# Kernel optimization log

Hardware: AMD Instinct MI355X
Metric: run time of the kernel (lower is better)

Reference implementation:

```python
import jax, jax.numpy as jnp
import numpy as np

B, MAX_N, MAX_E, MAX_BETA = 16, 512, 1024, 64
NODE_F, HID = 2, 128

def setup_inputs() -> dict:
    key = jax.random.key(0)
    ks = jax.random.split(key, 20)
    inp = {}
    inp["x"] = jax.random.normal(ks[0], (B, MAX_N, NODE_F), dtype=jnp.float32)
    inp["SCB"] = jax.random.normal(ks[1], (B, MAX_BETA, MAX_E), dtype=jnp.float32)
    inp["edge_index"] = jax.random.randint(ks[2], (B, 2, MAX_E), 0, MAX_N, dtype=jnp.int32)
    inp["edge_len"] = jax.random.randint(ks[3], (B,), 1, MAX_E + 1, dtype=jnp.int32)
    inp["beta_len"] = jax.random.randint(ks[4], (B,), 1, MAX_BETA + 1, dtype=jnp.int32)
    def lin(k, fi, fo):
        s = 1.0 / np.sqrt(fi)
        kw, kb = jax.random.split(k)
        return (jax.random.uniform(kw, (fi, fo), jnp.float32, -s, s),
                jax.random.uniform(kb, (fo,), jnp.float32, -s, s))
    inp["W1"], inp["b1"] = lin(ks[5], 4, 64)
    inp["W2"], inp["b2"] = lin(ks[6], 64, 64)
    inp["W3"], inp["b3"] = lin(ks[7], 64 + 4, 128)
    inp["W4"], inp["b4"] = lin(ks[8], 128, 128)
    inp["W5"], inp["b5"] = lin(ks[9], 128, HID)
    inp["W6"], inp["b6"] = lin(ks[10], HID, HID)
    return inp

def reference(x, SCB, edge_index, edge_len, beta_len,
              W1, b1, W2, b2, W3, b3, W4, b4, W5, b5, W6, b6):
    Bb, beta, E = SCB.shape
    SCBa = jnp.abs(SCB)  # torch.abs(he[2].to_dense())
    edge_mask = jnp.arange(E)[None, :] < edge_len[:, None]      # [B,E]
    beta_mask = jnp.arange(beta)[None, :] < beta_len[:, None]   # [B,beta]
    # e_feat = x[edge_index].transpose(0,1).reshape(E, 2*node_feat)
    ef = jax.vmap(lambda xi, ei: xi[ei])(x, edge_index)          # [B,2,E,F]
    ef = jnp.transpose(ef, (0, 2, 1, 3)).reshape(Bb, E, -1)      # [B,E,4]
    # SCB_feat[b,beta,e,i] = e_feat[b,e,i] * SCB[b,beta,e]; zero in padded region
    valid = (beta_mask[:, :, None] & edge_mask[:, None, :])[..., None]
    SCB_feat = jnp.where(valid, SCBa[:, :, :, None] * ef[:, None, :, :], 0.0)  # [B,beta,E,4]
    L1 = jnp.transpose(SCB_feat, (0, 2, 1, 3))                   # [B,E,beta,4]
    # SCB_encoder on sum over edges
    s = L1.sum(axis=1)                                            # [B,beta,4]
    emb = jax.nn.relu(s @ W1 + b1) @ W2 + b2                      # [B,beta,64]
    cat = jnp.concatenate([jnp.broadcast_to(emb[:, None], (Bb, E, beta, 64)), L1], axis=-1)
    h = (jax.nn.relu(cat @ W3 + b3) @ W4 + b4).sum(axis=2)        # [B,E,128]
    out = jax.nn.relu(h @ W5 + b5) @ W6 + b6                      # [B,E,HID]
    out = out.reshape(Bb * E, -1)
    # original selects out[Pad_Masks]; zero padded rows instead (jit-static shape)
    return out * edge_mask.reshape(-1, 1).astype(out.dtype)
```

## Files before the change

kernel.cpp:

```cpp
#include <hip/hip_runtime.h>
#include <hip/hip_bf16.h>

#define NB   16
#define NN   512
#define NE   1024
#define NBETA 64
#define NHID 128

typedef __attribute__((ext_vector_type(8))) short short8;
typedef __attribute__((ext_vector_type(4))) float f32x4;

static __device__ __forceinline__ unsigned short f2bf(float f) {
    unsigned u = __float_as_uint(f);
    return (unsigned short)((u + 0x7fffu + ((u >> 16) & 1u)) >> 16);
}

static __device__ __forceinline__ f32x4 splat4(float v) {
    f32x4 r; r.x = v; r.y = v; r.z = v; r.w = v; return r;
}


__global__ __launch_bounds__(512) void k_base_wt(
        const float* __restrict__ x, const int* __restrict__ ei,
        const float* __restrict__ SCB,
        const int* __restrict__ elen, const int* __restrict__ blen,
        const float* __restrict__ W1, const float* __restrict__ b1,
        const float* __restrict__ W2, const float* __restrict__ b2,
        const float* __restrict__ W3, const float* __restrict__ b3,
        const float* __restrict__ W4, const float* __restrict__ W5,
        const float* __restrict__ W6,
        float* __restrict__ base, unsigned short* __restrict__ wsT) {
    __shared__ float part[32];
    __shared__ float h1s[4][64];
    __shared__ float embs[4][64];
    int bid = blockIdx.x, tid = threadIdx.x;

    if (tid < 192) {
        int j = bid * 192 + tid;
        int w = j >> 14, rem = j & 16383;
        int k = rem & 127, n = rem >> 7;
        const float* W = (w == 0) ? W4 : ((w == 1) ? W5 : W6);
        float v = W[k * NHID + n];
        int byte = n * 256 + ((2 * k) ^ ((n & 7) << 4));
        *reinterpret_cast<unsigned short*>(
            reinterpret_cast<char*>(wsT) + (size_t)w * 32768 + byte) = f2bf(v);
    }

    int hf = tid >> 7, t = tid & 127;
    int bb = bid * 4 + hf;
    int b = bb >> 6, beta = bb & 63;
    int el = elen[b], bl = blen[b];
    float a0 = 0, a1 = 0, a2 = 0, a3 = 0;
    if (beta < bl) {
        const float* row = SCB + (size_t)bb * NE;
        const int* eis = ei + b * 2 * NE;
        const float* xb = x + b * NN * 2;
        for (int e = t; e < el; e += 128) {
            float tt = fabsf(row[e]);
            int s0 = eis[e], s1 = eis[NE + e];
            float2 v0 = *reinterpret_cast<const float2*>(xb + 2 * s0);
            float2 v1 = *reinterpret_cast<const float2*>(xb + 2 * s1);
            a0 = fmaf(tt, v0.x, a0);
            a1 = fmaf(tt, v0.y, a1);
            a2 = fmaf(tt, v1.x, a2);
            a3 = fmaf(tt, v1.y, a3);
        }
    }
    #pragma unroll
    for (int off = 32; off > 0; off >>= 1) {
        a0 += __shfl_down(a0, off);
        a1 += __shfl_down(a1, off);
        a2 += __shfl_down(a2, off);
        a3 += __shfl_down(a3, off);
    }
    if ((tid & 63) == 0) {
        int w8 = tid >> 6;
        part[w8 * 4 + 0] = a0; part[w8 * 4 + 1] = a1;
        part[w8 * 4 + 2] = a2; part[w8 * 4 + 3] = a3;
    }
    __syncthreads();
    if (t < 64) {
        float v = b1[t];
        #pragma unroll
        for (int i = 0; i < 4; ++i) {
            float si = part[(2 * hf) * 4 + i] + part[(2 * hf + 1) * 4 + i];
            v = fmaf(si, W1[i * 64 + t], v);
        }
        h1s[hf][t] = fmaxf(v, 0.f);
    }
    __syncthreads();
    if (t < 64) {
        float v = b2[t];
        #pragma unroll 8
        for (int k = 0; k < 64; ++k) v = fmaf(h1s[hf][k], W2[k * 64 + t], v);
        embs[hf][t] = v;
    }
    __syncthreads();
    {
        float v = b3[t];
        #pragma unroll 8
        for (int k = 0; k < 64; ++k) v = fmaf(embs[hf][k], W3[k * NHID + t], v);
        base[(size_t)bb * NHID + t] = v;
    }
}

__global__ __launch_bounds__(512) void k_fused(
        const float* __restrict__ x, const int* __restrict__ ei,
        const float* __restrict__ SCB,
        const int* __restrict__ elen, const int* __restrict__ blen,
        const float* __restrict__ W3,
        const float* __restrict__ base, const unsigned short* __restrict__ wsT,
        const float* __restrict__ b4, const float* __restrict__ b5,
        const float* __restrict__ b6,
        float* __restrict__ out) {
    int bid = blockIdx.x, tid = threadIdx.x;
    int b = bid & 15;
    int e0 = (bid >> 4) * 32;
    int el = elen[b];
    if (e0 >= el) {
        float4 z; z.x = 0.f; z.y = 0.f; z.z = 0.f; z.w = 0.f;
        float4* o4 = reinterpret_cast<float4*>(out) + (size_t)(b * NE + e0) * (NHID / 4);
        o4[tid] = z;
        o4[tid + 512] = z;
        return;
    }
    int bl = blen[b];

    __shared__ __align__(16) char lds[65536];
    float* baseS = reinterpret_cast<float*>(lds);
    char*  wS    = lds + 32768;
    float4* efS  = reinterpret_cast<float4*>(wS);
    float* w3r   = reinterpret_cast<float*>(wS + 512);
    float* tS    = reinterpret_cast<float*>(wS + 8192);
    char* io0 = lds;
    char* io1 = lds + 8192;

    const float4* w4src = reinterpret_cast<const float4*>(wsT);
    const float4* w5src = reinterpret_cast<const float4*>(
        reinterpret_cast<const char*>(wsT) + 32768);
    const float4* w6src = reinterpret_cast<const float4*>(
        reinterpret_cast<const char*>(wsT) + 65536);
    float4 pw0, pw1, pw2, pw3;

    {
        const float4* bsrc = reinterpret_cast<const float4*>(base + (size_t)b * NBETA * NHID);
        float4* bd = reinterpret_cast<float4*>(baseS);
        #pragma unroll
        for (int i = 0; i < 4; ++i) bd[tid + 512 * i] = bsrc[tid + 512 * i];
        {
            int row = tid >> 3, c4 = tid & 7;
            float4 v = *reinterpret_cast<const float4*>(
                SCB + (size_t)(b * NBETA + row) * NE + e0 + c4 * 4);
            v.x = fabsf(v.x); v.y = fabsf(v.y); v.z = fabsf(v.z); v.w = fabsf(v.w);
            reinterpret_cast<float4*>(tS)[tid] = v;
        }
        if (tid < 64) {
            int e = tid >> 1, hf = tid & 1;
            int idx = ei[b * 2 * NE + hf * NE + e0 + e];
            float2 v2 = *reinterpret_cast<const float2*>(x + b * NN * 2 + idx * 2);
            reinterpret_cast<float2*>(&efS[e])[hf] = v2;
        }
        w3r[tid] = W3[64 * NHID + tid];
        pw0 = w4src[tid];        pw1 = w4src[tid + 512];
        pw2 = w4src[tid + 1024]; pw3 = w4src[tid + 1536];
    }
    __syncthreads();

    int cg = tid & 31, es = tid >> 5;
    f32x4 w0  = reinterpret_cast<const f32x4*>(w3r)[cg];
    f32x4 w1  = reinterpret_cast<const f32x4*>(w3r)[32 + cg];
    f32x4 w2  = reinterpret_cast<const f32x4*>(w3r)[64 + cg];
    f32x4 w3v = reinterpret_cast<const f32x4*>(w3r)[96 + cg];
    f32x4 gv[2], acc[2];
    #pragma unroll
    for (int j = 0; j < 2; ++j) {
        float4 e4 = efS[es * 2 + j];
        f32x4 g = w3v * splat4(e4.w);
        g = __builtin_elementwise_fma(splat4(e4.z), w2, g);
        g = __builtin_elementwise_fma(splat4(e4.y), w1, g);
        g = __builtin_elementwise_fma(splat4(e4.x), w0, g);
        gv[j] = g;
        acc[j] = splat4(0.f);
    }
    const f32x4* base4 = reinterpret_cast<const f32x4*>(baseS);
    const f32x4 zero = splat4(0.f);
    for (int beta = 0; beta < bl; ++beta) {
        f32x4 bs = base4[beta * 32 + cg];
        float2 tv = *reinterpret_cast<const float2*>(tS + beta * 32 + es * 2);
        acc[0] += __builtin_elementwise_max(
            __builtin_elementwise_fma(splat4(tv.x), gv[0], bs), zero);
        acc[1] += __builtin_elementwise_max(
            __builtin_elementwise_fma(splat4(tv.y), gv[1], bs), zero);
    }
    if (bl < NBETA) {
        f32x4 bp = base4[bl * 32 + cg];
        f32x4 r = __builtin_elementwise_max(bp, zero);
        f32x4 fcv = splat4((float)(NBETA - bl));
        acc[0] = __builtin_elementwise_fma(fcv, r, acc[0]);
        acc[1] = __builtin_elementwise_fma(fcv, r, acc[1]);
    }
    __syncthreads();

    #pragma unroll
    for (int j = 0; j < 2; ++j) {
        int rl = es * 2 + j;
        int byte = rl * 256 + ((cg * 8) ^ ((rl & 7) << 4));
        ushort4 u;
        u.x = f2bf(acc[j].x); u.y = f2bf(acc[j].y);
        u.z = f2bf(acc[j].z); u.w = f2bf(acc[j].w);
        *reinterpret_cast<ushort4*>(io0 + byte) = u;
    }
    float4* wd = reinterpret_cast<float4*>(wS);
    wd[tid] = pw0; wd[tid + 512] = pw1; wd[tid + 1024] = pw2; wd[tid + 1536] = pw3;
    pw0 = w5src[tid];        pw1 = w5src[tid + 512];
    pw2 = w5src[tid + 1024]; pw3 = w5src[tid + 1536];
    __syncthreads();

    int l = tid & 63, wid = tid >> 6;
    int wm = wid & 1, wn = wid >> 1;
    const int lrow = l & 15;
    const int kbl = (l >> 4) * 16;

    auto layerc = [&](const char* ioIn, char* ioOut, const float* bias,
                      float bscale, bool doRelu, bool final_) {
        f32x4 facc[2];
        facc[0] = splat4(0.f); facc[1] = splat4(0.f);
        int rowA = wm * 16 + lrow;
        #pragma unroll
        for (int ks = 0; ks < 4; ++ks) {
            int kbyte = ks * 64 + kbl;
            short8 a = *reinterpret_cast<const short8*>(
                ioIn + rowA * 256 + (kbyte ^ ((rowA & 7) << 4)));
            #pragma unroll
            for (int nf = 0; nf < 2; ++nf) {
                int col = wn * 32 + nf * 16 + lrow;
                short8 bf = *reinterpret_cast<const short8*>(
                    wS + col * 256 + (kbyte ^ ((col & 7) << 4)));
                facc[nf] = __builtin_amdgcn_mfma_f32_16x16x32_bf16(a, bf, facc[nf], 0, 0, 0);
            }
        }
        #pragma unroll
        for (int nf = 0; nf < 2; ++nf) {
            int colg = wn * 32 + nf * 16 + lrow;
            float bvv = bias[colg];
            #pragma unroll
            for (int r = 0; r < 4; ++r) {
                int row = wm * 16 + (l >> 4) * 4 + r;
                float v = fmaf(bscale, bvv, facc[nf][r]);
                if (doRelu) v = fmaxf(v, 0.f);
                if (!final_) {
                    *reinterpret_cast<unsigned short*>(
                        ioOut + row * 256 + ((colg * 2) ^ ((row & 7) << 4))) = f2bf(v);
                } else {
                    int eg = e0 + row;
                    float vv = (eg >= el) ? 0.f : v;
                    out[(size_t)(b * NE + eg) * NHID + colg] = vv;
                }
            }
        }
    };

    layerc(io0, io1, b4, 64.f, false, false);
    __syncthreads();
    wd[tid] = pw0; wd[tid + 512] = pw1; wd[tid + 1024] = pw2; wd[tid + 1536] = pw3;
    pw0 = w6src[tid];        pw1 = w6src[tid + 512];
    pw2 = w6src[tid + 1024]; pw3 = w6src[tid + 1536];
    __syncthreads();
    layerc(io1, io0, b5, 1.f, true, false);
    __syncthreads();
    wd[tid] = pw0; wd[tid + 512] = pw1; wd[tid + 1024] = pw2; wd[tid + 1536] = pw3;
    __syncthreads();
    layerc(io0, nullptr, b6, 1.f, false, true);
}

extern "C" void kernel_launch(void* const* d_in, const int* in_sizes, int n_in,
                              void* d_out, int out_size, void* d_ws, size_t ws_size,
                              hipStream_t stream) {
    const float* x    = (const float*)d_in[0];
    const float* SCB  = (const float*)d_in[1];
    const int*   ei   = (const int*)d_in[2];
    const int*   elen = (const int*)d_in[3];
    const int*   blen = (const int*)d_in[4];
    const float* W1 = (const float*)d_in[5];  const float* b1 = (const float*)d_in[6];
    const float* W2 = (const float*)d_in[7];  const float* b2 = (const float*)d_in[8];
    const float* W3 = (const float*)d_in[9];  const float* b3 = (const float*)d_in[10];
    const float* W4 = (const float*)d_in[11]; const float* b4 = (const float*)d_in[12];
    const float* W5 = (const float*)d_in[13]; const float* b5 = (const float*)d_in[14];
    const float* W6 = (const float*)d_in[15]; const float* b6 = (const float*)d_in[16];
    float* out = (float*)d_out;

    float* ws = (float*)d_ws;
    float* base = ws;
    unsigned short* wsT = (unsigned short*)(base + NB * NBETA * NHID);

    hipLaunchKernelGGL(k_base_wt, dim3(256), dim3(512), 0, stream,
                       x, ei, SCB, elen, blen, W1, b1, W2, b2, W3, b3, W4, W5, W6, base, wsT);
    hipLaunchKernelGGL(k_fused, dim3(512), dim3(512), 0, stream,
                       x, ei, SCB, elen, blen, W3, base, wsT, b4, b5, b6, out);
}
```

Baseline: 26.99 us.

## Fuse base/emb computation into single kernel with 64-edge tiles and MFMA encoders

```diff
diff --git a/kernel.cpp b/kernel.cpp
--- a/kernel.cpp
+++ b/kernel.cpp
@@ -14,217 +14,313 @@
     unsigned u = __float_as_uint(f);
     return (unsigned short)((u + 0x7fffu + ((u >> 16) & 1u)) >> 16);
 }
-
+static __device__ __forceinline__ unsigned packbf2(float lo, float hi) {
+    return (unsigned)f2bf(lo) | ((unsigned)f2bf(hi) << 16);
+}
 static __device__ __forceinline__ f32x4 splat4(float v) {
     f32x4 r; r.x = v; r.y = v; r.z = v; r.w = v; return r;
 }
 
-
-__global__ __launch_bounds__(512) void k_base_wt(
+__global__ __launch_bounds__(512) void k_one(
         const float* __restrict__ x, const int* __restrict__ ei,
         const float* __restrict__ SCB,
         const int* __restrict__ elen, const int* __restrict__ blen,
         const float* __restrict__ W1, const float* __restrict__ b1,
         const float* __restrict__ W2, const float* __restrict__ b2,
         const float* __restrict__ W3, const float* __restrict__ b3,
-        const float* __restrict__ W4, const float* __restrict__ W5,
-        const float* __restrict__ W6,
-        float* __restrict__ base, unsigned short* __restrict__ wsT) {
-    __shared__ float part[32];
-    __shared__ float h1s[4][64];
-    __shared__ float embs[4][64];
-    int bid = blockIdx.x, tid = threadIdx.x;
-
-    if (tid < 192) {
-        int j = bid * 192 + tid;
-        int w = j >> 14, rem = j & 16383;
-        int k = rem & 127, n = rem >> 7;
-        const float* W = (w == 0) ? W4 : ((w == 1) ? W5 : W6);
-        float v = W[k * NHID + n];
-        int byte = n * 256 + ((2 * k) ^ ((n & 7) << 4));
-        *reinterpret_cast<unsigned short*>(
-            reinterpret_cast<char*>(wsT) + (size_t)w * 32768 + byte) = f2bf(v);
-    }
-
-    int hf = tid >> 7, t = tid & 127;
-    int bb = bid * 4 + hf;
-    int b = bb >> 6, beta = bb & 63;
-    int el = elen[b], bl = blen[b];
-    float a0 = 0, a1 = 0, a2 = 0, a3 = 0;
-    if (beta < bl) {
-        const float* row = SCB + (size_t)bb * NE;
-        const int* eis = ei + b * 2 * NE;
-        const float* xb = x + b * NN * 2;
-        for (int e = t; e < el; e += 128) {
-            float tt = fabsf(row[e]);
-            int s0 = eis[e], s1 = eis[NE + e];
-            float2 v0 = *reinterpret_cast<const float2*>(xb + 2 * s0);
-            float2 v1 = *reinterpret_cast<const float2*>(xb + 2 * s1);
-            a0 = fmaf(tt, v0.x, a0);
-            a1 = fmaf(tt, v0.y, a1);
-            a2 = fmaf(tt, v1.x, a2);
-            a3 = fmaf(tt, v1.y, a3);
-        }
-    }
-    #pragma unroll
-    for (int off = 32; off > 0; off >>= 1) {
-        a0 += __shfl_down(a0, off);
-        a1 += __shfl_down(a1, off);
-        a2 += __shfl_down(a2, off);
-        a3 += __shfl_down(a3, off);
-    }
-    if ((tid & 63) == 0) {
-        int w8 = tid >> 6;
-        part[w8 * 4 + 0] = a0; part[w8 * 4 + 1] = a1;
-        part[w8 * 4 + 2] = a2; part[w8 * 4 + 3] = a3;
-    }
-    __syncthreads();
-    if (t < 64) {
-        float v = b1[t];
-        #pragma unroll
-        for (int i = 0; i < 4; ++i) {
-            float si = part[(2 * hf) * 4 + i] + part[(2 * hf + 1) * 4 + i];
-            v = fmaf(si, W1[i * 64 + t], v);
-        }
-        h1s[hf][t] = fmaxf(v, 0.f);
-    }
-    __syncthreads();
-    if (t < 64) {
-        float v = b2[t];
-        #pragma unroll 8
-        for (int k = 0; k < 64; ++k) v = fmaf(h1s[hf][k], W2[k * 64 + t], v);
-        embs[hf][t] = v;
-    }
-    __syncthreads();
-    {
-        float v = b3[t];
-        #pragma unroll 8
-        for (int k = 0; k < 64; ++k) v = fmaf(embs[hf][k], W3[k * NHID + t], v);
-        base[(size_t)bb * NHID + t] = v;
-    }
-}
-
-__global__ __launch_bounds__(512) void k_fused(
-        const float* __restrict__ x, const int* __restrict__ ei,
-        const float* __restrict__ SCB,
-        const int* __restrict__ elen, const int* __restrict__ blen,
-        const float* __restrict__ W3,
-        const float* __restrict__ base, const unsigned short* __restrict__ wsT,
-        const float* __restrict__ b4, const float* __restrict__ b5,
-        const float* __restrict__ b6,
+        const float* __restrict__ W4, const float* __restrict__ b4,
+        const float* __restrict__ W5, const float* __restrict__ b5,
+        const float* __restrict__ W6, const float* __restrict__ b6,
         float* __restrict__ out) {
+    __shared__ __align__(16) char lds[65536];
+    char* r0 = lds;
+    char* r1 = lds + 32768;
     int bid = blockIdx.x, tid = threadIdx.x;
     int b = bid & 15;
-    int e0 = (bid >> 4) * 32;
+    int e0 = (bid >> 4) * 64;
     int el = elen[b];
     if (e0 >= el) {
         float4 z; z.x = 0.f; z.y = 0.f; z.z = 0.f; z.w = 0.f;
-        float4* o4 = reinterpret_cast<float4*>(out) + (size_t)(b * NE + e0) * (NHID / 4);
-        o4[tid] = z;
-        o4[tid + 512] = z;
+        float4* o4 = reinterpret_cast<float4*>(out) + (size_t)(b * NE + e0) * 32;
+        #pragma unroll
+        for (int q = 0; q < 4; ++q) o4[tid + 512 * q] = z;
         return;
     }
     int bl = blen[b];
 
-    __shared__ __align__(16) char lds[65536];
-    float* baseS = reinterpret_cast<float*>(lds);
-    char*  wS    = lds + 32768;
-    float4* efS  = reinterpret_cast<float4*>(wS);
-    float* w3r   = reinterpret_cast<float*>(wS + 512);
-    float* tS    = reinterpret_cast<float*>(wS + 8192);
-    char* io0 = lds;
-    char* io1 = lds + 8192;
-
-    const float4* w4src = reinterpret_cast<const float4*>(wsT);
-    const float4* w5src = reinterpret_cast<const float4*>(
-        reinterpret_cast<const char*>(wsT) + 32768);
-    const float4* w6src = reinterpret_cast<const float4*>(
-        reinterpret_cast<const char*>(wsT) + 65536);
-    float4 pw0, pw1, pw2, pw3;
-
-    {
-        const float4* bsrc = reinterpret_cast<const float4*>(base + (size_t)b * NBETA * NHID);
-        float4* bd = reinterpret_cast<float4*>(baseS);
-        #pragma unroll
-        for (int i = 0; i < 4; ++i) bd[tid + 512 * i] = bsrc[tid + 512 * i];
+    float*  efAT = reinterpret_cast<float*>(r1);
+    float*  w3r  = reinterpret_cast<float*>(r1 + 16384);
+    f32x4*  sS4  = reinterpret_cast<f32x4*>(r1 + 18432);
+    float4* tS4  = reinterpret_cast<float4*>(r0);
+    char* w2b  = r0 + 16384;
+    char* h1a  = r0 + 24576;
+    char* w3b  = r1;
+    char* emba = r0 + 16384;
+    float* baseS = reinterpret_cast<float*>(r1);
+    char* io0 = r0;
+    char* io1 = r0 + 16384;
+    char* wS  = r1;
+
+    {
+        const int* eib = ei + b * 2 * NE;
+        const float* xb = x + b * NN * 2;
+        for (int e = tid; e < NE; e += 512) {
+            int i0 = eib[e], i1 = eib[NE + e];
+            float2 v0 = *reinterpret_cast<const float2*>(xb + 2 * i0);
+            float2 v1 = *reinterpret_cast<const float2*>(xb + 2 * i1);
+            efAT[e] = v0.x; efAT[1024 + e] = v0.y;
+            efAT[2048 + e] = v1.x; efAT[3072 + e] = v1.y;
+        }
+        const float4* scb4 = reinterpret_cast<const float4*>(
+            SCB + (size_t)(b * NBETA) * NE);
+        for (int i = tid; i < 1024; i += 512) {
+            int row = i >> 4, c4 = i & 15;
+            float4 v = scb4[row * 256 + (e0 >> 2) + c4];
+            v.x = fabsf(v.x); v.y = fabsf(v.y); v.z = fabsf(v.z); v.w = fabsf(v.w);
+            tS4[i] = v;
+        }
+        w3r[tid] = W3[64 * NHID + tid];
         {
-            int row = tid >> 3, c4 = tid & 7;
-            float4 v = *reinterpret_cast<const float4*>(
-                SCB + (size_t)(b * NBETA + row) * NE + e0 + c4 * 4);
-            v.x = fabsf(v.x); v.y = fabsf(v.y); v.z = fabsf(v.z); v.w = fabsf(v.w);
-            reinterpret_cast<float4*>(tS)[tid] = v;
-        }
-        if (tid < 64) {
-            int e = tid >> 1, hf = tid & 1;
-            int idx = ei[b * 2 * NE + hf * NE + e0 + e];
-            float2 v2 = *reinterpret_cast<const float2*>(x + b * NN * 2 + idx * 2);
-            reinterpret_cast<float2*>(&efS[e])[hf] = v2;
-        }
-        w3r[tid] = W3[64 * NHID + tid];
-        pw0 = w4src[tid];        pw1 = w4src[tid + 512];
-        pw2 = w4src[tid + 1024]; pw3 = w4src[tid + 1536];
-    }
-    __syncthreads();
-
-    int cg = tid & 31, es = tid >> 5;
-    f32x4 w0  = reinterpret_cast<const f32x4*>(w3r)[cg];
-    f32x4 w1  = reinterpret_cast<const f32x4*>(w3r)[32 + cg];
-    f32x4 w2  = reinterpret_cast<const f32x4*>(w3r)[64 + cg];
-    f32x4 w3v = reinterpret_cast<const f32x4*>(w3r)[96 + cg];
-    f32x4 gv[2], acc[2];
+            int c = tid >> 4, n4 = tid & 15;
+            float4 lo = *reinterpret_cast<const float4*>(W2 + (2 * c) * 64 + n4 * 4);
+            float4 hi = *reinterpret_cast<const float4*>(W2 + (2 * c + 1) * 64 + n4 * 4);
+            #pragma unroll
+            for (int m = 0; m < 4; ++m) {
+                int n = n4 * 4 + m;
+                *reinterpret_cast<unsigned*>(
+                    w2b + n * 128 + ((4 * c) ^ ((n & 7) << 4))) =
+                    packbf2(((const float*)&lo)[m], ((const float*)&hi)[m]);
+            }
+        }
+    }
+    __syncthreads();
+
+    int cg = tid & 31, slot = tid >> 5;
+    f32x4 gv[4];
+    {
+        f32x4 w0  = reinterpret_cast<const f32x4*>(w3r)[cg];
+        f32x4 w1v = reinterpret_cast<const f32x4*>(w3r)[32 + cg];
+        f32x4 w2v = reinterpret_cast<const f32x4*>(w3r)[64 + cg];
+        f32x4 w3v = reinterpret_cast<const f32x4*>(w3r)[96 + cg];
+        #pragma unroll
+        for (int j = 0; j < 4; ++j) {
+            int e = e0 + slot * 4 + j;
+            f32x4 g = w3v * splat4(efAT[3072 + e]);
+            g = __builtin_elementwise_fma(splat4(efAT[2048 + e]), w2v, g);
+            g = __builtin_elementwise_fma(splat4(efAT[1024 + e]), w1v, g);
+            g = __builtin_elementwise_fma(splat4(efAT[e]), w0, g);
+            gv[j] = g;
+        }
+    }
+
+    {
+        int beta = tid >> 3, j = tid & 7;
+        f32x4 sacc = splat4(0.f);
+        if (beta < bl) {
+            const float4* row4 = reinterpret_cast<const float4*>(
+                SCB + (size_t)(b * NBETA + beta) * NE);
+            for (int k = 0; k < 32; ++k) {
+                int f = j + 8 * k, e = 4 * f;
+                float4 c4 = row4[f];
+                float m0 = (e     < el) ? fabsf(c4.x) : 0.f;
+                float m1 = (e + 1 < el) ? fabsf(c4.y) : 0.f;
+                float m2 = (e + 2 < el) ? fabsf(c4.z) : 0.f;
+                float m3 = (e + 3 < el) ? fabsf(c4.w) : 0.f;
+                #pragma unroll
+                for (int i = 0; i < 4; ++i) {
+                    const float* efi = efAT + i * 1024 + e;
+                    float v = sacc[i];
+                    v = fmaf(m0, efi[0], v);
+                    v = fmaf(m1, efi[1], v);
+                    v = fmaf(m2, efi[2], v);
+                    v = fmaf(m3, efi[3], v);
+                    sacc[i] = v;
+                }
+            }
+        }
+        #pragma unroll
+        for (int off = 4; off > 0; off >>= 1) {
+            sacc[0] += __shfl_down(sacc[0], off);
+            sacc[1] += __shfl_down(sacc[1], off);
+            sacc[2] += __shfl_down(sacc[2], off);
+            sacc[3] += __shfl_down(sacc[3], off);
+        }
+        if (j == 0) sS4[beta] = sacc;
+    }
+    __syncthreads();
+
+    {
+        int beta = tid >> 3, c0 = (tid & 7) * 8;
+        f32x4 sv = sS4[beta];
+        float h[8];
+        #pragma unroll
+        for (int cc = 0; cc < 8; ++cc) {
+            int c = c0 + cc;
+            float v = b1[c];
+            v = fmaf(sv[0], W1[c], v);
+            v = fmaf(sv[1], W1[64 + c], v);
+            v = fmaf(sv[2], W1[128 + c], v);
+            v = fmaf(sv[3], W1[192 + c], v);
+            h[cc] = fmaxf(v, 0.f);
+        }
+        #pragma unroll
+        for (int p = 0; p < 4; ++p) {
+            int c = c0 + 2 * p;
+            *reinterpret_cast<unsigned*>(
+                h1a + beta * 128 + ((2 * c) ^ ((beta & 7) << 4))) =
+                packbf2(h[2 * p], h[2 * p + 1]);
+        }
+        int cw = tid >> 5, n4 = tid & 31;
+        #pragma unroll
+        for (int q = 0; q < 2; ++q) {
+            int c = cw + 16 * q;
+            float4 lo = *reinterpret_cast<const float4*>(W3 + (2 * c) * NHID + n4 * 4);
+            float4 hi = *reinterpret_cast<const float4*>(W3 + (2 * c + 1) * NHID + n4 * 4);
+            #pragma unroll
+            for (int m = 0; m < 4; ++m) {
+                int n = n4 * 4 + m;
+                *reinterpret_cast<unsigned*>(
+                    w3b + n * 128 + ((4 * c) ^ ((n & 7) << 4))) =
+                    packbf2(((const float*)&lo)[m], ((const float*)&hi)[m]);
+            }
+        }
+    }
+    __syncthreads();
+
+    int l = tid & 63, wid = tid >> 6;
+    const int lrow = l & 15;
+    const int kbl = (l >> 4) * 16;
+
+    {
+        int wm = wid & 3, wn = wid >> 2;
+        f32x4 ef[2];
+        ef[0] = splat4(0.f); ef[1] = splat4(0.f);
+        int rowA = wm * 16 + lrow;
+        #pragma unroll
+        for (int ks = 0; ks < 2; ++ks) {
+            int kbyte = ks * 64 + kbl;
+            short8 a = *reinterpret_cast<const short8*>(
+                h1a + rowA * 128 + (kbyte ^ ((rowA & 7) << 4)));
+            #pragma unroll
+            for (int nf = 0; nf < 2; ++nf) {
+                int col = wn * 32 + nf * 16 + lrow;
+                short8 bf = *reinterpret_cast<const short8*>(
+                    w2b + col * 128 + (kbyte ^ ((col & 7) << 4)));
+                ef[nf] = __builtin_amdgcn_mfma_f32_16x16x32_bf16(a, bf, ef[nf], 0, 0, 0);
+            }
+        }
+        __syncthreads();
+        #pragma unroll
+        for (int nf = 0; nf < 2; ++nf) {
+            int colg = wn * 32 + nf * 16 + lrow;
+            float bv = b2[colg];
+            #pragma unroll
+            for (int r = 0; r < 4; ++r) {
+                int beta = wm * 16 + (l >> 4) * 4 + r;
+                *reinterpret_cast<unsigned short*>(
+                    emba + beta * 128 + ((2 * colg) ^ ((beta & 7) << 4))) =
+                    f2bf(ef[nf][r] + bv);
+            }
+        }
+    }
+    __syncthreads();
+
+    {
+        int wm = wid & 3, wn = wid >> 2;
+        f32x4 bf4[4];
+        #pragma unroll
+        for (int nf = 0; nf < 4; ++nf) bf4[nf] = splat4(0.f);
+        int rowA = wm * 16 + lrow;
+        #pragma unroll
+        for (int ks = 0; ks < 2; ++ks) {
+            int kbyte = ks * 64 + kbl;
+            short8 a = *reinterpret_cast<const short8*>(
+                emba + rowA * 128 + (kbyte ^ ((rowA & 7) << 4)));
+            #pragma unroll
+            for (int nf = 0; nf < 4; ++nf) {
+                int col = wn * 64 + nf * 16 + lrow;
+                short8 bfr = *reinterpret_cast<const short8*>(
+                    w3b + col * 128 + (kbyte ^ ((col & 7) << 4)));
+                bf4[nf] = __builtin_amdgcn_mfma_f32_16x16x32_bf16(a, bfr, bf4[nf], 0, 0, 0);
+            }
+        }
+        __syncthreads();
+        #pragma unroll
+        for (int nf = 0; nf < 4; ++nf) {
+            int colg = wn * 64 + nf * 16 + lrow;
+            float bv = b3[colg];
+            #pragma unroll
+            for (int r = 0; r < 4; ++r) {
+                int beta = wm * 16 + (l >> 4) * 4 + r;
+                baseS[beta * NHID + colg] = bf4[nf][r] + bv;
+            }
+        }
+    }
+    __syncthreads();
+
+    f32x4 acc[4];
     #pragma unroll
-    for (int j = 0; j < 2; ++j) {
-        float4 e4 = efS[es * 2 + j];
-        f32x4 g = w3v * splat4(e4.w);
-        g = __builtin_elementwise_fma(splat4(e4.z), w2, g);
-        g = __builtin_elementwise_fma(splat4(e4.y), w1, g);
-        g = __builtin_elementwise_fma(splat4(e4.x), w0, g);
-        gv[j] = g;
-        acc[j] = splat4(0.f);
-    }
-    const f32x4* base4 = reinterpret_cast<const f32x4*>(baseS);
-    const f32x4 zero = splat4(0.f);
-    for (int beta = 0; beta < bl; ++beta) {
-        f32x4 bs = base4[beta * 32 + cg];
-        float2 tv = *reinterpret_cast<const float2*>(tS + beta * 32 + es * 2);
-        acc[0] += __builtin_elementwise_max(
-            __builtin_elementwise_fma(splat4(tv.x), gv[0], bs), zero);
-        acc[1] += __builtin_elementwise_max(
-            __builtin_elementwise_fma(splat4(tv.y), gv[1], bs), zero);
-    }
-    if (bl < NBETA) {
-        f32x4 bp = base4[bl * 32 + cg];
-        f32x4 r = __builtin_elementwise_max(bp, zero);
-        f32x4 fcv = splat4((float)(NBETA - bl));
-        acc[0] = __builtin_elementwise_fma(fcv, r, acc[0]);
-        acc[1] = __builtin_elementwise_fma(fcv, r, acc[1]);
+    for (int j = 0; j < 4; ++j) acc[j] = splat4(0.f);
+    {
+        const f32x4* base4 = reinterpret_cast<const f32x4*>(baseS);
+        const f32x4 zero = splat4(0.f);
+        for (int beta = 0; beta < bl; ++beta) {
+            f32x4 bs = base4[beta * 32 + cg];
+            float4 tv = tS4[beta * 16 + slot];
+            acc[0] += __builtin_elementwise_max(
+                __builtin_elementwise_fma(splat4(tv.x), gv[0], bs), zero);
+            acc[1] += __builtin_elementwise_max(
+                __builtin_elementwise_fma(splat4(tv.y), gv[1], bs), zero);
+            acc[2] += __builtin_elementwise_max(
+                __builtin_elementwise_fma(splat4(tv.z), gv[2], bs), zero);
+            acc[3] += __builtin_elementwise_max(
+                __builtin_elementwise_fma(splat4(tv.w), gv[3], bs), zero);
+        }
+        if (bl < NBETA) {
+            f32x4 bp = base4[bl * 32 + cg];
+            f32x4 r = __builtin_elementwise_max(bp, zero);
+            f32x4 fcv = splat4((float)(NBETA - bl));
+            #pragma unroll
+            for (int j = 0; j < 4; ++j)
+                acc[j] = __builtin_elementwise_fma(fcv, r, acc[j]);
+        }
     }
     __syncthreads();
 
     #pragma unroll
-    for (int j = 0; j < 2; ++j) {
-        int rl = es * 2 + j;
+    for (int j = 0; j < 4; ++j) {
+        int rl = slot * 4 + j;
         int byte = rl * 256 + ((cg * 8) ^ ((rl & 7) << 4));
         ushort4 u;
         u.x = f2bf(acc[j].x); u.y = f2bf(acc[j].y);
         u.z = f2bf(acc[j].z); u.w = f2bf(acc[j].w);
         *reinterpret_cast<ushort4*>(io0 + byte) = u;
     }
-    float4* wd = reinterpret_cast<float4*>(wS);
-    wd[tid] = pw0; wd[tid + 512] = pw1; wd[tid + 1024] = pw2; wd[tid + 1536] = pw3;
-    pw0 = w5src[tid];        pw1 = w5src[tid + 512];
-    pw2 = w5src[tid + 1024]; pw3 = w5src[tid + 1536];
-    __syncthreads();
-
-    int l = tid & 63, wid = tid >> 6;
-    int wm = wid & 1, wn = wid >> 1;
-    const int lrow = l & 15;
-    const int kbl = (l >> 4) * 16;
+    auto commitW = [&](const float* Wg) {
+        int c0 = tid >> 5, n4 = tid & 31;
+        #pragma unroll
+        for (int q = 0; q < 4; ++q) {
+            int c = c0 + 16 * q;
+            float4 lo = *reinterpret_cast<const float4*>(Wg + (2 * c) * NHID + n4 * 4);
+            float4 hi = *reinterpret_cast<const float4*>(Wg + (2 * c + 1) * NHID + n4 * 4);
+            #pragma unroll
+            for (int m = 0; m < 4; ++m) {
+                int n = n4 * 4 + m;
+                *reinterpret_cast<unsigned*>(
+                    wS + n * 256 + ((4 * c) ^ ((n & 7) << 4))) =
+                    packbf2(((const float*)&lo)[m], ((const float*)&hi)[m]);
+            }
+        }
+    };
+    commitW(W4);
+    __syncthreads();
 
     auto layerc = [&](const char* ioIn, char* ioOut, const float* bias,
                       float bscale, bool doRelu, bool final_) {
-        f32x4 facc[2];
-        facc[0] = splat4(0.f); facc[1] = splat4(0.f);
+        int wm = wid & 3, wn = wid >> 2;
+        f32x4 facc[4];
+        #pragma unroll
+        for (int nf = 0; nf < 4; ++nf) facc[nf] = splat4(0.f);
         int rowA = wm * 16 + lrow;
         #pragma unroll
         for (int ks = 0; ks < 4; ++ks) {
@@ -232,16 +328,16 @@
             short8 a = *reinterpret_cast<const short8*>(
                 ioIn + rowA * 256 + (kbyte ^ ((rowA & 7) << 4)));
             #pragma unroll
-            for (int nf = 0; nf < 2; ++nf) {
-                int col = wn * 32 + nf * 16 + lrow;
-                short8 bf = *reinterpret_cast<const short8*>(
+            for (int nf = 0; nf < 4; ++nf) {
+                int col = wn * 64 + nf * 16 + lrow;
+                short8 bfr = *reinterpret_cast<const short8*>(
                     wS + col * 256 + (kbyte ^ ((col & 7) << 4)));
-                facc[nf] = __builtin_amdgcn_mfma_f32_16x16x32_bf16(a, bf, facc[nf], 0, 0, 0);
-            }
-        }
-        #pragma unroll
-        for (int nf = 0; nf < 2; ++nf) {
-            int colg = wn * 32 + nf * 16 + lrow;
+                facc[nf] = __builtin_amdgcn_mfma_f32_16x16x32_bf16(a, bfr, facc[nf], 0, 0, 0);
+            }
+        }
+        #pragma unroll
+        for (int nf = 0; nf < 4; ++nf) {
+            int colg = wn * 64 + nf * 16 + lrow;
             float bvv = bias[colg];
             #pragma unroll
             for (int r = 0; r < 4; ++r) {
@@ -262,13 +358,11 @@
 
     layerc(io0, io1, b4, 64.f, false, false);
     __syncthreads();
-    wd[tid] = pw0; wd[tid + 512] = pw1; wd[tid + 1024] = pw2; wd[tid + 1536] = pw3;
-    pw0 = w6src[tid];        pw1 = w6src[tid + 512];
-    pw2 = w6src[tid + 1024]; pw3 = w6src[tid + 1536];
+    commitW(W5);
     __syncthreads();
     layerc(io1, io0, b5, 1.f, true, false);
     __syncthreads();
-    wd[tid] = pw0; wd[tid + 512] = pw1; wd[tid + 1024] = pw2; wd[tid + 1536] = pw3;
+    commitW(W6);
     __syncthreads();
     layerc(io0, nullptr, b6, 1.f, false, true);
 }
@@ -289,12 +383,7 @@
     const float* W6 = (const float*)d_in[15]; const float* b6 = (const float*)d_in[16];
     float* out = (float*)d_out;
 
-    float* ws = (float*)d_ws;
-    float* base = ws;
-    unsigned short* wsT = (unsigned short*)(base + NB * NBETA * NHID);
-
-    hipLaunchKernelGGL(k_base_wt, dim3(256), dim3(512), 0, stream,
-                       x, ei, SCB, elen, blen, W1, b1, W2, b2, W3, b3, W4, W5, W6, base, wsT);
-    hipLaunchKernelGGL(k_fused, dim3(512), dim3(512), 0, stream,
-                       x, ei, SCB, elen, blen, W3, base, wsT, b4, b5, b6, out);
-}
+    hipLaunchKernelGGL(k_one, dim3(256), dim3(512), 0, stream,
+                       x, ei, SCB, elen, blen, W1, b1, W2, b2, W3, b3,
+                       W4, b4, W5, b5, W6, b6, out);
+}
```

New measurement: 88.37 us. 227% more time.
